# Kernel tuning notes

Measured on AMD Instinct MI355X. Metric: run time of the kernel, lower is better.

The kernel has to match this reference:

```python
import jax, jax.numpy as jnp
import numpy as np


def _lin(x, w, b=None):
    # torch nn.Linear convention: y = x @ W^T + b, W: (out, in)
    y = jnp.einsum('...d,ed->...e', x, w)
    return y + b if b is not None else y


def setup_inputs() -> dict:
    key = jax.random.key(0)
    B, N, M, d = 8, 256, 128, 128
    ks = jax.random.split(key, 20)
    sc = 1.0 / np.sqrt(d)
    inp = {
        's': jax.random.normal(ks[0], (B, N, d), jnp.float32),
        'v': jax.random.normal(ks[1], (B, N, M, d), jnp.float32),
        'gs': jax.random.normal(ks[2], (B, d), jnp.float32),
        'gv': jax.random.normal(ks[3], (B, M, d), jnp.float32),
        'gv2': jax.random.normal(ks[4], (B, M, M, d), jnp.float32),
        'lin1_w': jax.random.normal(ks[5], (d, d), jnp.float32) * sc,
        'lin1_b': jax.random.normal(ks[6], (d,), jnp.float32) * sc,
        'lin2_w': jax.random.normal(ks[7], (d, d), jnp.float32) * sc,
        'lin2_b': jax.random.normal(ks[8], (d,), jnp.float32) * sc,
        'lin3_w': jax.random.normal(ks[9], (d, d), jnp.float32) * sc,
        'lin3_b': jax.random.normal(ks[10], (d,), jnp.float32) * sc,
        'linv1_w': jax.random.normal(ks[11], (d, d), jnp.float32) * sc,
        'linv2_w': jax.random.normal(ks[12], (d, d), jnp.float32) * sc,
        'linv3_w': jax.random.normal(ks[13], (d, d), jnp.float32) * sc,
        'mlp_w1': jax.random.normal(ks[14], (d, d), jnp.float32) * sc,
        'mlp_b1': jax.random.normal(ks[15], (d,), jnp.float32) * sc,
        'mlp_w2': jax.random.normal(ks[16], (d, d), jnp.float32) * sc,
        'mlp_b2': jax.random.normal(ks[17], (d,), jnp.float32) * sc,
    }
    return inp


def reference(s, v, gs, gv, gv2,
              lin1_w, lin1_b, lin2_w, lin2_b, lin3_w, lin3_b,
              linv1_w, linv2_w, linv3_w,
              mlp_w1, mlp_b1, mlp_w2, mlp_b2):
    # v update: three (B,N,M,d) branches, averaged
    v_vv2 = _lin(jnp.einsum('bnmd,bmcd->bncd', v, gv2), linv1_w)
    v_vs = _lin(gs[:, None, None, :] * v, linv3_w)
    v_sv = _lin(s[:, :, None, :] * gv[:, None, :, :], linv2_w)
    v_new = (v_vv2 + v_sv + v_vs) / 3
    # s update
    s_v2t = jnp.einsum('bmmd->bd', gv2)                 # per-channel trace of gv2
    s_vv = jnp.einsum('bmd,bnmd->bnd', gv, v_new)
    s_new = ((_lin(s_v2t, lin1_w, lin1_b) * gs)[:, None, :]
             * _lin(s, lin2_w, lin2_b)
             * _lin(s_vv, lin3_w, lin3_b))
    # MLP: Linear -> ReLU -> Linear
    s_new = _lin(jax.nn.relu(_lin(s_new, mlp_w1, mlp_b1)), mlp_w2, mlp_b2)
    return (s_new, v_new)
```

## Files before the change

### kernel.cpp

```cpp
#include <hip/hip_runtime.h>
#include <hip/hip_bf16.h>
#include <stdint.h>

#define B_ 8
#define N_ 256
#define M_ 128
#define D_ 128

typedef __attribute__((ext_vector_type(8))) short short8;
typedef __attribute__((ext_vector_type(4))) short short4v;
typedef __attribute__((ext_vector_type(4))) float f32x4;

static __device__ __forceinline__ unsigned short f2bf(float x) {
    union { float f; unsigned int u; } c; c.f = x;
    unsigned int r = (c.u + 0x7FFFu + ((c.u >> 16) & 1u)) >> 16;
    return (unsigned short)r;
}
static __device__ __forceinline__ unsigned short bfhu(float x) {
    union { float f; unsigned int u; } c; c.f = x;
    return (unsigned short)((c.u + 0x8000u) >> 16);
}
static __device__ __forceinline__ unsigned int pkhu(float a, float b) {
    union { float f; unsigned int u; } ca, cb; ca.f = a; cb.f = b;
    return ((ca.u + 0x8000u) >> 16) | ((cb.u + 0x8000u) & 0xFFFF0000u);
}
static __device__ __forceinline__ float4 mul4(float4 a, float4 b) {
    return make_float4(a.x * b.x, a.y * b.y, a.z * b.z, a.w * b.w);
}
static __device__ __forceinline__ short8 pack8(float4 a, float4 b) {
    return (short8){(short)f2bf(a.x), (short)f2bf(a.y), (short)f2bf(a.z), (short)f2bf(a.w),
                    (short)f2bf(b.x), (short)f2bf(b.y), (short)f2bf(b.z), (short)f2bf(b.w)};
}

__global__ void k0a_prep(const float* __restrict__ lin2_w, const float* __restrict__ lin3_w,
                         const float* __restrict__ mlp_w1, const float* __restrict__ mlp_w2,
                         const float* __restrict__ linv1_w, const float* __restrict__ linv2_w,
                         const float* __restrict__ linv3_w,
                         float* __restrict__ wT2, float* __restrict__ wT3,
                         float* __restrict__ wTm1, float* __restrict__ wTm2,
                         unsigned short* __restrict__ wfrag) {
    int gid = blockIdx.x * 256 + threadIdx.x;
    int task = gid >> 14;
    int idx = gid & 16383;
    if (task < 4) {
        int e = idx & 127, dd = idx >> 7;
        const float* src = task == 0 ? lin2_w : task == 1 ? lin3_w : task == 2 ? mlp_w1 : mlp_w2;
        float* dst = task == 0 ? wT2 : task == 1 ? wT3 : task == 2 ? wTm1 : wTm2;
        dst[dd * 128 + e] = src[e * 128 + dd];
    } else {
        int mat = task - 4;
        const float* src = mat == 0 ? linv1_w : mat == 1 ? linv2_w : linv3_w;
        int e = idx >> 7, k = idx & 127;
        int dst = ((((e >> 4) * 12 + (mat * 4 + (k >> 5))) * 4 + ((k >> 3) & 3)) * 16 + (e & 15)) * 8
                  + (k & 7);
        wfrag[dst] = f2bf(src[idx] * (1.0f / 3.0f));
    }
}

__global__ void k0b_trace(const float* __restrict__ gv2, float* __restrict__ s_v2t) {
    int b = blockIdx.x, d = threadIdx.x;
    const float* p = gv2 + (size_t)b * (M_ * M_ * D_) + d;
    float acc = 0.f;
    #pragma unroll 8
    for (int m = 0; m < 128; ++m) acc += p[(size_t)m * 16512];
    s_v2t[b * 128 + d] = acc;
}

__global__ void k0c_g1(const float* __restrict__ s_v2t, const float* __restrict__ lin1_w,
                       const float* __restrict__ lin1_b, const float* __restrict__ gs,
                       float* __restrict__ g1) {
    __shared__ float sv[128];
    int b = blockIdx.x, e = threadIdx.x;
    sv[e] = s_v2t[b * 128 + e];
    __syncthreads();
    const float* w = lin1_w + e * 128;
    float acc = 0.f;
    #pragma unroll 4
    for (int dd = 0; dd < 128; ++dd) acc = fmaf(sv[dd], w[dd], acc);
    g1[b * 128 + e] = (acc + lin1_b[e]) * gs[b * 128 + e];
}

__global__ __launch_bounds__(256) void kt_v(const float* __restrict__ v,
                                            unsigned short* __restrict__ vT) {
    __shared__ unsigned short tl[128 * 136];
    int bid = blockIdx.x;
    int b = bid >> 8;
    int R0 = (bid & 255) * 128;
    int t = threadIdx.x;
    const float* src = v + ((size_t)b * 32768 + R0) * 128;
    #pragma unroll
    for (int i = 0; i < 16; ++i) {
        int flat = i * 256 + t;
        int row = flat >> 5, slot = flat & 31;
        float4 x = *(const float4*)(src + (size_t)row * 128 + slot * 4);
        #pragma unroll
        for (int j = 0; j < 4; ++j) {
            int d = slot * 4 + j;
            tl[d * 136 + (row ^ (((d >> 2) & 7) << 3))] = bfhu(((const float*)&x)[j]);
        }
    }
    __syncthreads();
    #pragma unroll
    for (int i = 0; i < 8; ++i) {
        int flat = i * 256 + t;
        int d = flat >> 4, rs = flat & 15;
        short8 y = *(const short8*)&tl[d * 136 + ((rs * 8) ^ (((d >> 2) & 7) << 3))];
        *(short8*)(vT + (size_t)(b * 128 + d) * 32768 + R0 + rs * 8) = y;
    }
}

__global__ __launch_bounds__(256) void kt_g(const float* __restrict__ gv2,
                                            unsigned short* __restrict__ gT) {
    __shared__ unsigned short tl[128 * 136];
    int bid = blockIdx.x;
    int b = bid >> 7;
    int c = bid & 127;
    int t = threadIdx.x;
    const float* src = gv2 + ((size_t)(b * 128) * 128 + c) * 128;
    #pragma unroll
    for (int i = 0; i < 16; ++i) {
        int flat = i * 256 + t;
        int m = flat >> 5, slot = flat & 31;
        float4 x = *(const float4*)(src + (size_t)m * 16384 + slot * 4);
        #pragma unroll
        for (int j = 0; j < 4; ++j) {
            int d = slot * 4 + j;
            tl[d * 136 + (m ^ (((d >> 2) & 7) << 3))] = bfhu(((const float*)&x)[j]);
        }
    }
    __syncthreads();
    #pragma unroll
    for (int i = 0; i < 8; ++i) {
        int flat = i * 256 + t;
        int d = flat >> 4, ms = flat & 15;
        short8 y = *(const short8*)&tl[d * 136 + ((ms * 8) ^ (((d >> 2) & 7) << 3))];
        *(short8*)(gT + ((size_t)(b * 128 + d) * 128 + c) * 128 + ms * 8) = y;
    }
}

__global__ __launch_bounds__(512, 2) void k1_T2_fast(const unsigned short* __restrict__ vT,
                                                     const unsigned short* __restrict__ gT,
                                                     unsigned short* __restrict__ t2base) {
    __shared__ unsigned short sm[40960];
    int bid = blockIdx.x;
    int b = bid & 7;
    int r = bid >> 3;
    int nt = r & 3, ch = (r >> 2) & 1, dc = r >> 3;
    int n0 = nt * 64, c0 = ch * 64, d0 = dc * 8;
    int t = threadIdx.x;
    int w = t >> 6, lane = t & 63, ln15 = lane & 15, kg = lane >> 4;

    f32x4 acc[4][4];
    #pragma unroll
    for (int i = 0; i < 4; ++i)
        #pragma unroll
        for (int j = 0; j < 4; ++j) acc[i][j] = (f32x4){0.f, 0.f, 0.f, 0.f};

    for (int mc = 0; mc < 4; ++mc) {
        int m0 = mc * 32;
        #pragma unroll
        for (int i = 0; i < 4; ++i) {
            int flat = i * 512 + t;
            int d = flat >> 8, x = (flat >> 2) & 63, ms = flat & 3;
            short8 a = *(const short8*)(vT + ((size_t)(b * 128 + d0 + d) * 256 + n0 + x) * 128
                                           + m0 + ms * 8);
            *(short8*)&sm[d * 2560 + x * 40 + ms * 8] = a;
            short8 g = *(const short8*)(gT + ((size_t)(b * 128 + d0 + d) * 128 + c0 + x) * 128
                                           + m0 + ms * 8);
            *(short8*)&sm[20480 + d * 2560 + x * 40 + ms * 8] = g;
        }
        __syncthreads();
        short8 af[4], bf[4];
        #pragma unroll
        for (int i = 0; i < 4; ++i)
            af[i] = *(const short8*)&sm[w * 2560 + (i * 16 + ln15) * 40 + kg * 8];
        #pragma unroll
        for (int j = 0; j < 4; ++j)
            bf[j] = *(const short8*)&sm[20480 + w * 2560 + (j * 16 + ln15) * 40 + kg * 8];
        #pragma unroll
        for (int i = 0; i < 4; ++i)
            #pragma unroll
            for (int j = 0; j < 4; ++j)
                acc[i][j] = __builtin_amdgcn_mfma_f32_16x16x32_bf16(af[i], bf[j], acc[i][j], 0, 0, 0);
        __syncthreads();
    }
    #pragma unroll
    for (int i = 0; i < 4; ++i)
        #pragma unroll
        for (int j = 0; j < 4; ++j)
            #pragma unroll
            for (int q = 0; q < 4; ++q) {
                int n = i * 16 + kg * 4 + q;
                int c = j * 16 + ln15;
                sm[n * 520 + c * 8 + w] = bfhu(acc[i][j][q]);
            }
    __syncthreads();
    #pragma unroll
    for (int p = 0; p < 8; ++p) {
        int u = p * 512 + t;
        int n = u >> 6;
        int c = u & 63;
        short8 x = *(const short8*)&sm[n * 520 + c * 8];
        size_t kb = (size_t)(b * N_ + n0 + n) * 2 + ch;
        *(short8*)(t2base + kb * 16384 + (size_t)((c >> 4) * 16 + dc) * 128 + (c & 15) * 8) = x;
    }
}

__global__ __launch_bounds__(512, 4) void k1_T2_legacy(const float* __restrict__ v,
                                                       const float* __restrict__ gv2,
                                                       unsigned short* __restrict__ t2base) {
    __shared__ unsigned short sm[40960];
    int bid = blockIdx.x;
    int b = bid & 7;
    int r = bid >> 3;
    int nt = r & 3, ch = (r >> 2) & 1, dc = r >> 3;
    int n0 = nt * 64, c0 = ch * 64, d0 = dc * 8;
    int t = threadIdx.x;
    int w = t >> 6, lane = t & 63, ln15 = lane & 15, kg = lane >> 4;

    f32x4 acc[4][4];
    #pragma unroll
    for (int i = 0; i < 4; ++i)
        #pragma unroll
        for (int j = 0; j < 4; ++j) acc[i][j] = (f32x4){0.f, 0.f, 0.f, 0.f};

    int d0l = (t & 1) * 4;
    int am = (t >> 1) & 31, anb = t >> 6;
    int bc = (t >> 1) & 63, bmb = t >> 7;

    for (int mc = 0; mc < 4; ++mc) {
        int m0 = mc * 32;
        {
            const float* src = v + (((size_t)(b * N_ + n0) * M_ + m0 + am) * D_ + d0 + d0l);
            #pragma unroll
            for (int p = 0; p < 8; ++p) {
                int n = p * 8 + anb;
                float4 x = *(const float4*)(src + (size_t)n * (M_ * D_));
                #pragma unroll
                for (int j = 0; j < 4; ++j)
                    sm[(d0l + j) * 2560 + n * 40 + am] = f2bf(((const float*)&x)[j]);
            }
        }
        {
            const float* src = gv2 + (((size_t)(b * M_ + m0) * M_ + c0 + bc) * D_ + d0 + d0l);
            #pragma unroll
            for (int p = 0; p < 8; ++p) {
                int m = p * 4 + bmb;
                float4 x = *(const float4*)(src + (size_t)m * (M_ * D_));
                #pragma unroll
                for (int j = 0; j < 4; ++j)
                    sm[20480 + (d0l + j) * 2560 + bc * 40 + m] = f2bf(((const float*)&x)[j]);
            }
        }
        __syncthreads();
        short8 af[4], bf[4];
        #pragma unroll
        for (int i = 0; i < 4; ++i)
            af[i] = *(const short8*)&sm[w * 2560 + (i * 16 + ln15) * 40 + kg * 8];
        #pragma unroll
        for (int j = 0; j < 4; ++j)
            bf[j] = *(const short8*)&sm[20480 + w * 2560 + (j * 16 + ln15) * 40 + kg * 8];
        #pragma unroll
        for (int i = 0; i < 4; ++i)
            #pragma unroll
            for (int j = 0; j < 4; ++j)
                acc[i][j] = __builtin_amdgcn_mfma_f32_16x16x32_bf16(af[i], bf[j], acc[i][j], 0, 0, 0);
        __syncthreads();
    }
    #pragma unroll
    for (int i = 0; i < 4; ++i)
        #pragma unroll
        for (int j = 0; j < 4; ++j)
            #pragma unroll
            for (int q = 0; q < 4; ++q) {
                int n = i * 16 + kg * 4 + q;
                int c = j * 16 + ln15;
                sm[(n * 64 + c) * 8 + w] = f2bf(acc[i][j][q]);
            }
    __syncthreads();
    #pragma unroll
    for (int p = 0; p < 8; ++p) {
        int u = p * 512 + t;
        int n = u >> 6;
        int c = u & 63;
        short8 x = *(const short8*)&sm[(n * 64 + c) * 8];
        size_t kb = (size_t)(b * N_ + n0 + n) * 2 + ch;
        *(short8*)(t2base + kb * 16384 + (size_t)((c >> 4) * 16 + dc) * 128 + (c & 15) * 8) = x;
    }
}

__global__ __launch_bounds__(512, 2) void k2_vnew(
        const float* __restrict__ s, const float* __restrict__ v,
        const float* __restrict__ gs, const float* __restrict__ gv,
        const unsigned short* __restrict__ wfrag,
        float* __restrict__ vnew, float* __restrict__ svv) {
    __shared__ unsigned short smw[49152];
    __shared__ float part[2][4][128];
    int t = threadIdx.x;
    int w = t >> 6;
    int sb = w >> 2;
    int w4 = w & 3;
    int kb2 = blockIdx.x * 2 + sb;
    int b = kb2 >> 8;
    int lane = t & 63, ln15 = lane & 15, kgrp = lane >> 4;

    #pragma unroll
    for (int r = 0; r < 12; ++r) {
        int idx = (r * 512 + t) * 8;
        *(short8*)&smw[idx] = *(const short8*)(wfrag + idx);
    }
    const unsigned short* t2u = (const unsigned short*)(vnew + (size_t)kb2 * 16384);
    short8 aT[2][4];
    #pragma unroll
    for (int h = 0; h < 2; ++h) {
        int rt = w4 * 2 + h;
        const unsigned short* tb = t2u + (rt >> 2) * 16384 + ((rt & 3) * 16 + kgrp) * 128 + ln15 * 8;
        #pragma unroll
        for (int kk = 0; kk < 4; ++kk)
            aT[h][kk] = *(const short8*)(tb + kk * 512);
    }
    const float* srow = s + (size_t)kb2 * 128;
    const float* gsr  = gs + (size_t)b * 128;
    float4 ss[8], qq[8];
    #pragma unroll
    for (int kk = 0; kk < 4; ++kk) {
        int dd = kk * 32 + kgrp * 8;
        ss[kk * 2]     = *(const float4*)(srow + dd);
        ss[kk * 2 + 1] = *(const float4*)(srow + dd + 4);
        qq[kk * 2]     = *(const float4*)(gsr + dd);
        qq[kk * 2 + 1] = *(const float4*)(gsr + dd + 4);
    }
    __syncthreads();

    float psum[8] = {0.f, 0.f, 0.f, 0.f, 0.f, 0.f, 0.f, 0.f};
    #pragma unroll
    for (int h = 0; h < 2; ++h) {
        int rt = w4 * 2 + h;
        int ca = rt * 16 + ln15;
        const float* gvr = gv + ((size_t)b * M_ + ca) * D_;
        const float* vr  = v + ((size_t)kb2 * M_ + ca) * D_;
        short8 aD[8];
        #pragma unroll
        for (int kk = 0; kk < 4; ++kk) {
            int dd = kk * 32 + kgrp * 8;
            float4 g0 = *(const float4*)(gvr + dd), g1 = *(const float4*)(gvr + dd + 4);
            float4 v0 = *(const float4*)(vr + dd),  v1 = *(const float4*)(vr + dd + 4);
            aD[kk]     = pack8(mul4(ss[kk * 2], g0), mul4(ss[kk * 2 + 1], g1));
            aD[4 + kk] = pack8(mul4(qq[kk * 2], v0), mul4(qq[kk * 2 + 1], v1));
        }
        float* outp = vnew + (size_t)kb2 * 16384 + (rt >> 2) * 8192;
        int rowl = (rt & 3) * 16 + kgrp * 4;
        const float* grow = gv + ((size_t)b * M_ + rt * 16 + kgrp * 4) * D_;
        #pragma unroll
        for (int ct = 0; ct < 8; ++ct) {
            f32x4 acc = {0.f, 0.f, 0.f, 0.f};
            #pragma unroll
            for (int kk = 0; kk < 12; ++kk) {
                short8 a = (kk < 4) ? aT[h][kk] : aD[kk - 4];
                short8 bfr = *(const short8*)&smw[(((ct * 12 + kk) * 4 + kgrp) * 16 + ln15) * 8];
                acc = __builtin_amdgcn_mfma_f32_16x16x32_bf16(a, bfr, acc, 0, 0, 0);
            }
            int e = ct * 16 + ln15;
            #pragma unroll
            for (int q = 0; q < 4; ++q) {
                outp[(size_t)(rowl + q) * 128 + e] = acc[q];
                psum[ct] = fmaf(grow[(size_t)q * 128 + e], acc[q], psum[ct]);
            }
        }
    }
    #pragma unroll
    for (int ct = 0; ct < 8; ++ct) {
        psum[ct] += __shfl_xor(psum[ct], 16);
        psum[ct] += __shfl_xor(psum[ct], 32);
    }
    if (kgrp == 0) {
        #pragma unroll
        for (int ct = 0; ct < 8; ++ct) part[sb][w4][ct * 16 + ln15] = psum[ct];
    }
    __syncthreads();
    int tl = t & 255;
    int sb2 = t >> 8;
    if (tl < 128) {
        int kbo = blockIdx.x * 2 + sb2;
        svv[(size_t)kbo * 128 + tl] =
            part[sb2][0][tl] + part[sb2][1][tl] + part[sb2][2][tl] + part[sb2][3][tl];
    }
}

__global__ __launch_bounds__(256) void k4_spath(
        const float* __restrict__ s, const float* __restrict__ svv,
        const float* __restrict__ g1,
        const float* __restrict__ wT2, const float* __restrict__ lin2_b,
        const float* __restrict__ wT3, const float* __restrict__ lin3_b,
        const float* __restrict__ wTm1, const float* __restrict__ mlp_b1,
        const float* __restrict__ wTm2, const float* __restrict__ mlp_b2,
        float* __restrict__ sout) {
    __shared__ float xs[8][128], xv[8][128], pre[8][128], hbuf[8][128];
    int t = threadIdx.x;
    int rowb = blockIdx.x * 8;
    int b = rowb >> 8;
    #pragma unroll
    for (int i = 0; i < 4; ++i) {
        int vi = i * 256 + t;
        int r = vi >> 7, dd = vi & 127;
        xs[r][dd] = s[(size_t)(rowb + r) * 128 + dd];
        xv[r][dd] = svv[(size_t)(rowb + r) * 128 + dd];
    }
    __syncthreads();
    int e = t & 127, h2 = t >> 7;
    float b2 = lin2_b[e], b3 = lin3_b[e], g1v = g1[b * 128 + e];
    float a2[4] = {b2, b2, b2, b2}, a3[4] = {b3, b3, b3, b3};
    for (int dd = 0; dd < 128; ++dd) {
        float w2 = wT2[dd * 128 + e], w3 = wT3[dd * 128 + e];
        #pragma unroll
        for (int r = 0; r < 4; ++r) {
            a2[r] = fmaf(xs[h2 * 4 + r][dd], w2, a2[r]);
            a3[r] = fmaf(xv[h2 * 4 + r][dd], w3, a3[r]);
        }
    }
    #pragma unroll
    for (int r = 0; r < 4; ++r) pre[h2 * 4 + r][e] = g1v * a2[r] * a3[r];
    __syncthreads();
    float bm1 = mlp_b1[e];
    float ah[4] = {bm1, bm1, bm1, bm1};
    for (int dd = 0; dd < 128; ++dd) {
        float w = wTm1[dd * 128 + e];
        #pragma unroll
        for (int r = 0; r < 4; ++r) ah[r] = fmaf(pre[h2 * 4 + r][dd], w, ah[r]);
    }
    #pragma unroll
    for (int r = 0; r < 4; ++r) hbuf[h2 * 4 + r][e] = fmaxf(ah[r], 0.f);
    __syncthreads();
    float bm2 = mlp_b2[e];
    float ao[4] = {bm2, bm2, bm2, bm2};
    for (int dd = 0; dd < 128; ++dd) {
        float w = wTm2[dd * 128 + e];
        #pragma unroll
        for (int r = 0; r < 4; ++r) ao[r] = fmaf(hbuf[h2 * 4 + r][dd], w, ao[r]);
    }
    #pragma unroll
    for (int r = 0; r < 4; ++r) sout[(size_t)(rowb + h2 * 4 + r) * 128 + e] = ao[r];
}

extern "C" void kernel_launch(void* const* d_in, const int* in_sizes, int n_in,
                              void* d_out, int out_size, void* d_ws, size_t ws_size,
                              hipStream_t stream) {
    const float* s       = (const float*)d_in[0];
    const float* v       = (const float*)d_in[1];
    const float* gs      = (const float*)d_in[2];
    const float* gv      = (const float*)d_in[3];
    const float* gv2     = (const float*)d_in[4];
    const float* lin1_w  = (const float*)d_in[5];
    const float* lin1_b  = (const float*)d_in[6];
    const float* lin2_w  = (const float*)d_in[7];
    const float* lin2_b  = (const float*)d_in[8];
    const float* lin3_w  = (const float*)d_in[9];
    const float* lin3_b  = (const float*)d_in[10];
    const float* linv1_w = (const float*)d_in[11];
    const float* linv2_w = (const float*)d_in[12];
    const float* linv3_w = (const float*)d_in[13];
    const float* mlp_w1  = (const float*)d_in[14];
    const float* mlp_b1  = (const float*)d_in[15];
    const float* mlp_w2  = (const float*)d_in[16];
    const float* mlp_b2  = (const float*)d_in[17];

    float* sout = (float*)d_out;
    float* vnew = (float*)d_out + 262144;

    float* wsf   = (float*)d_ws;
    float* wT2   = wsf;
    float* wT3   = wsf + 16384;
    float* wTm1  = wsf + 32768;
    float* wTm2  = wsf + 49152;
    float* s_v2t = wsf + 65536;
    float* g1    = wsf + 66560;
    float* svv   = wsf + 67584;
    unsigned short* wfrag = (unsigned short*)(wsf + 329728);
    unsigned short* vT = (unsigned short*)((char*)d_ws + 2097152);
    unsigned short* gT = (unsigned short*)((char*)d_ws + 69206016);
    bool big = ws_size >= 102760448ULL;

    k0a_prep<<<448, 256, 0, stream>>>(lin2_w, lin3_w, mlp_w1, mlp_w2,
                                      linv1_w, linv2_w, linv3_w,
                                      wT2, wT3, wTm1, wTm2, wfrag);
    k0b_trace<<<8, 128, 0, stream>>>(gv2, s_v2t);
    k0c_g1<<<8, 128, 0, stream>>>(s_v2t, lin1_w, lin1_b, gs, g1);
    if (big) {
        kt_v<<<2048, 256, 0, stream>>>(v, vT);
        kt_g<<<1024, 256, 0, stream>>>(gv2, gT);
        k1_T2_fast<<<1024, 512, 0, stream>>>(vT, gT, (unsigned short*)vnew);
    } else {
        k1_T2_legacy<<<1024, 512, 0, stream>>>(v, gv2, (unsigned short*)vnew);
    }
    k2_vnew<<<1024, 512, 0, stream>>>(s, v, gs, gv, wfrag, vnew, svv);
    k4_spath<<<256, 256, 0, stream>>>(s, svv, g1, wT2, lin2_b, wT3, lin3_b,
                                      wTm1, mlp_b1, wTm2, mlp_b2, sout);
}
```

Baseline: 263.2 us.

## Precompute bf16 gs*v in transpose kernel and use persistent k2 kernel

The v transpose kernel now also writes a bf16 copy of gs*v in row-major layout. A new persistent k2 variant loads the weight fragments into shared memory once per block and loops over four work pairs, reading the half-size bf16 gs*v instead of fp32 v. It only runs when the workspace is large enough. This aims to cut v read traffic in k2 and the repeated weight staging, at the cost of an extra 64MB bf16 write in kt_v and lower occupancy (256 blocks, launch bound 1).

New measurement: 276.8 us. 5.2% more time.

```diff
diff --git a/kernel.cpp b/kernel.cpp
--- a/kernel.cpp
+++ b/kernel.cpp
@@ -81,22 +81,31 @@
 }
 
 __global__ __launch_bounds__(256) void kt_v(const float* __restrict__ v,
-                                            unsigned short* __restrict__ vT) {
+                                            const float* __restrict__ gs,
+                                            unsigned short* __restrict__ vT,
+                                            unsigned short* __restrict__ vgs) {
     __shared__ unsigned short tl[128 * 136];
     int bid = blockIdx.x;
     int b = bid >> 8;
     int R0 = (bid & 255) * 128;
     int t = threadIdx.x;
+    int slot = t & 31;
     const float* src = v + ((size_t)b * 32768 + R0) * 128;
+    float4 gs4 = *(const float4*)(gs + b * 128 + slot * 4);
     #pragma unroll
     for (int i = 0; i < 16; ++i) {
         int flat = i * 256 + t;
-        int row = flat >> 5, slot = flat & 31;
+        int row = flat >> 5;
         float4 x = *(const float4*)(src + (size_t)row * 128 + slot * 4);
         #pragma unroll
         for (int j = 0; j < 4; ++j) {
             int d = slot * 4 + j;
             tl[d * 136 + (row ^ (((d >> 2) & 7) << 3))] = bfhu(((const float*)&x)[j]);
+        }
+        if (vgs) {
+            uint2 pg = make_uint2(pkhu(x.x * gs4.x, x.y * gs4.y),
+                                  pkhu(x.z * gs4.z, x.w * gs4.w));
+            *(uint2*)(vgs + ((size_t)b * 32768 + R0 + row) * 128 + slot * 4) = pg;
         }
     }
     __syncthreads();
@@ -286,6 +295,102 @@
         short8 x = *(const short8*)&sm[(n * 64 + c) * 8];
         size_t kb = (size_t)(b * N_ + n0 + n) * 2 + ch;
         *(short8*)(t2base + kb * 16384 + (size_t)((c >> 4) * 16 + dc) * 128 + (c & 15) * 8) = x;
+    }
+}
+
+__global__ __launch_bounds__(512, 1) void k2_vnew_p(
+        const float* __restrict__ s, const unsigned short* __restrict__ vgs,
+        const float* __restrict__ gv,
+        const unsigned short* __restrict__ wfrag,
+        float* __restrict__ vnew, float* __restrict__ svv) {
+    __shared__ unsigned short smw[49152];
+    __shared__ float part[2][4][128];
+    int t = threadIdx.x;
+    int w = t >> 6, sb = w >> 2, w4 = w & 3;
+    int lane = t & 63, ln15 = lane & 15, kgrp = lane >> 4;
+
+    #pragma unroll
+    for (int r = 0; r < 12; ++r) {
+        int idx = (r * 512 + t) * 8;
+        *(short8*)&smw[idx] = *(const short8*)(wfrag + idx);
+    }
+
+    for (int j = 0; j < 4; ++j) {
+        int pair = blockIdx.x + 256 * j;
+        int kb2 = pair * 2 + sb;
+        int b = kb2 >> 8;
+        const unsigned short* t2u = (const unsigned short*)(vnew + (size_t)kb2 * 16384);
+        short8 aT[2][4];
+        #pragma unroll
+        for (int h = 0; h < 2; ++h) {
+            int rt = w4 * 2 + h;
+            const unsigned short* tb = t2u + (rt >> 2) * 16384 + ((rt & 3) * 16 + kgrp) * 128
+                                      + ln15 * 8;
+            #pragma unroll
+            for (int kk = 0; kk < 4; ++kk)
+                aT[h][kk] = *(const short8*)(tb + kk * 512);
+        }
+        const float* srow = s + (size_t)kb2 * 128;
+        float4 ss[8];
+        #pragma unroll
+        for (int kk = 0; kk < 4; ++kk) {
+            int dd = kk * 32 + kgrp * 8;
+            ss[kk * 2]     = *(const float4*)(srow + dd);
+            ss[kk * 2 + 1] = *(const float4*)(srow + dd + 4);
+        }
+        __syncthreads();
+
+        float psum[8] = {0.f, 0.f, 0.f, 0.f, 0.f, 0.f, 0.f, 0.f};
+        #pragma unroll
+        for (int h = 0; h < 2; ++h) {
+            int rt = w4 * 2 + h;
+            int ca = rt * 16 + ln15;
+            const float* gvr = gv + ((size_t)b * M_ + ca) * D_;
+            const unsigned short* vgr = vgs + ((size_t)kb2 * M_ + ca) * D_;
+            short8 aD[8];
+            #pragma unroll
+            for (int kk = 0; kk < 4; ++kk) {
+                int dd = kk * 32 + kgrp * 8;
+                float4 g0 = *(const float4*)(gvr + dd), g1 = *(const float4*)(gvr + dd + 4);
+                aD[kk]     = pack8(mul4(ss[kk * 2], g0), mul4(ss[kk * 2 + 1], g1));
+                aD[4 + kk] = *(const short8*)(vgr + dd);
+            }
+            float* outp = vnew + (size_t)kb2 * 16384 + (rt >> 2) * 8192;
+            int rowl = (rt & 3) * 16 + kgrp * 4;
+            const float* grow = gv + ((size_t)b * M_ + rt * 16 + kgrp * 4) * D_;
+            #pragma unroll
+            for (int ct = 0; ct < 8; ++ct) {
+                f32x4 acc = {0.f, 0.f, 0.f, 0.f};
+                #pragma unroll
+                for (int kk = 0; kk < 12; ++kk) {
+                    short8 a = (kk < 4) ? aT[h][kk] : aD[kk - 4];
+                    short8 bfr = *(const short8*)&smw[(((ct * 12 + kk) * 4 + kgrp) * 16 + ln15) * 8];
+                    acc = __builtin_amdgcn_mfma_f32_16x16x32_bf16(a, bfr, acc, 0, 0, 0);
+                }
+                int e = ct * 16 + ln15;
+                #pragma unroll
+                for (int q = 0; q < 4; ++q) {
+                    outp[(size_t)(rowl + q) * 128 + e] = acc[q];
+                    psum[ct] = fmaf(grow[(size_t)q * 128 + e], acc[q], psum[ct]);
+                }
+            }
+        }
+        #pragma unroll
+        for (int ct = 0; ct < 8; ++ct) {
+            psum[ct] += __shfl_xor(psum[ct], 16);
+            psum[ct] += __shfl_xor(psum[ct], 32);
+        }
+        if (kgrp == 0) {
+            #pragma unroll
+            for (int ct = 0; ct < 8; ++ct) part[sb][w4][ct * 16 + ln15] = psum[ct];
+        }
+        __syncthreads();
+        int tl = t & 255, sb2 = t >> 8;
+        if (tl < 128) {
+            int kbo = pair * 2 + sb2;
+            svv[(size_t)kbo * 128 + tl] =
+                part[sb2][0][tl] + part[sb2][1][tl] + part[sb2][2][tl] + part[sb2][3][tl];
+        }
     }
 }
 
@@ -476,9 +581,11 @@
     float* g1    = wsf + 66560;
     float* svv   = wsf + 67584;
     unsigned short* wfrag = (unsigned short*)(wsf + 329728);
-    unsigned short* vT = (unsigned short*)((char*)d_ws + 2097152);
-    unsigned short* gT = (unsigned short*)((char*)d_ws + 69206016);
-    bool big = ws_size >= 102760448ULL;
+    unsigned short* vT  = (unsigned short*)((char*)d_ws + 2097152);
+    unsigned short* gT  = (unsigned short*)((char*)d_ws + 69206016);
+    unsigned short* vgs = (unsigned short*)((char*)d_ws + 102760448);
+    bool big  = ws_size >= 102760448ULL;
+    bool huge = ws_size >= 169869312ULL;
 
     k0a_prep<<<448, 256, 0, stream>>>(lin2_w, lin3_w, mlp_w1, mlp_w2,
                                       linv1_w, linv2_w, linv3_w,
@@ -486,13 +593,17 @@
     k0b_trace<<<8, 128, 0, stream>>>(gv2, s_v2t);
     k0c_g1<<<8, 128, 0, stream>>>(s_v2t, lin1_w, lin1_b, gs, g1);
     if (big) {
-        kt_v<<<2048, 256, 0, stream>>>(v, vT);
+        kt_v<<<2048, 256, 0, stream>>>(v, gs, vT, huge ? vgs : (unsigned short*)nullptr);
         kt_g<<<1024, 256, 0, stream>>>(gv2, gT);
         k1_T2_fast<<<1024, 512, 0, stream>>>(vT, gT, (unsigned short*)vnew);
     } else {
         k1_T2_legacy<<<1024, 512, 0, stream>>>(v, gv2, (unsigned short*)vnew);
     }
-    k2_vnew<<<1024, 512, 0, stream>>>(s, v, gs, gv, wfrag, vnew, svv);
+    if (huge) {
+        k2_vnew_p<<<256, 512, 0, stream>>>(s, vgs, gv, wfrag, vnew, svv);
+    } else {
+        k2_vnew<<<1024, 512, 0, stream>>>(s, v, gs, gv, wfrag, vnew, svv);
+    }
     k4_spath<<<256, 256, 0, stream>>>(s, svv, g1, wT2, lin2_b, wT3, lin3_b,
                                       wTm1, mlp_b1, wTm2, mlp_b2, sout);
 }
```

## Restructure v_new kernel to keep weight fragments in registers and stage A in LDS

Applied to the files above, without the earlier changes.

The v_new projection kernel is rewritten so each block handles a single (b,n) row. Each wave owns one 16-wide output column tile and keeps its 12 weight fragments in registers, so the 96KB LDS weight copy goes away. The A operands (the T2 tile plus the s·gv and gs·v products) are now built cooperatively in a small LDS buffer, one row tile at a time. Row tiles are processed in a permuted order so that reading the in-place T2 buffer does not collide with writing v_new. The aim is higher occupancy and less LDS pressure, at the cost of two barriers per row tile and twice as many blocks.

Result: no change. 258.9 us (-1.6%).

```diff
diff --git a/kernel.cpp b/kernel.cpp
--- a/kernel.cpp
+++ b/kernel.cpp
@@ -23,13 +23,6 @@
 static __device__ __forceinline__ unsigned int pkhu(float a, float b) {
     union { float f; unsigned int u; } ca, cb; ca.f = a; cb.f = b;
     return ((ca.u + 0x8000u) >> 16) | ((cb.u + 0x8000u) & 0xFFFF0000u);
-}
-static __device__ __forceinline__ float4 mul4(float4 a, float4 b) {
-    return make_float4(a.x * b.x, a.y * b.y, a.z * b.z, a.w * b.w);
-}
-static __device__ __forceinline__ short8 pack8(float4 a, float4 b) {
-    return (short8){(short)f2bf(a.x), (short)f2bf(a.y), (short)f2bf(a.z), (short)f2bf(a.w),
-                    (short)f2bf(b.x), (short)f2bf(b.y), (short)f2bf(b.z), (short)f2bf(b.w)};
 }
 
 __global__ void k0a_prep(const float* __restrict__ lin2_w, const float* __restrict__ lin3_w,
@@ -289,102 +282,77 @@
     }
 }
 
-__global__ __launch_bounds__(512, 2) void k2_vnew(
+__global__ __launch_bounds__(512, 4) void k2_vnew_w(
         const float* __restrict__ s, const float* __restrict__ v,
         const float* __restrict__ gs, const float* __restrict__ gv,
         const unsigned short* __restrict__ wfrag,
         float* __restrict__ vnew, float* __restrict__ svv) {
-    __shared__ unsigned short smw[49152];
-    __shared__ float part[2][4][128];
-    int t = threadIdx.x;
-    int w = t >> 6;
-    int sb = w >> 2;
-    int w4 = w & 3;
-    int kb2 = blockIdx.x * 2 + sb;
+    __shared__ unsigned short lds_a[6144];
+    int t = threadIdx.x;
+    int kb2 = blockIdx.x;
     int b = kb2 >> 8;
-    int lane = t & 63, ln15 = lane & 15, kgrp = lane >> 4;
-
-    #pragma unroll
-    for (int r = 0; r < 12; ++r) {
-        int idx = (r * 512 + t) * 8;
-        *(short8*)&smw[idx] = *(const short8*)(wfrag + idx);
-    }
+    int w = t >> 6, lane = t & 63, ln15 = lane & 15, kgrp = lane >> 4;
+    int ct = w;
+
+    f32x4 wreg[12];
+    #pragma unroll
+    for (int kk = 0; kk < 12; ++kk)
+        wreg[kk] = *(const f32x4*)&wfrag[(((ct * 12 + kk) * 4 + kgrp) * 16 + ln15) * 8];
+    asm volatile("" : "+v"(wreg[0]), "+v"(wreg[1]), "+v"(wreg[2]), "+v"(wreg[3]),
+                      "+v"(wreg[4]), "+v"(wreg[5]), "+v"(wreg[6]), "+v"(wreg[7]),
+                      "+v"(wreg[8]), "+v"(wreg[9]), "+v"(wreg[10]), "+v"(wreg[11]));
+
+    int r_s = t >> 5;
+    int q5 = t & 31;
+    int dd0 = q5 * 4;
+    float4 s4  = *(const float4*)(s + (size_t)kb2 * 128 + dd0);
+    float4 gs4 = *(const float4*)(gs + (size_t)b * 128 + dd0);
+    const float* gvb = gv + (size_t)b * 16384;
     const unsigned short* t2u = (const unsigned short*)(vnew + (size_t)kb2 * 16384);
-    short8 aT[2][4];
-    #pragma unroll
-    for (int h = 0; h < 2; ++h) {
-        int rt = w4 * 2 + h;
-        const unsigned short* tb = t2u + (rt >> 2) * 16384 + ((rt & 3) * 16 + kgrp) * 128 + ln15 * 8;
-        #pragma unroll
-        for (int kk = 0; kk < 4; ++kk)
-            aT[h][kk] = *(const short8*)(tb + kk * 512);
-    }
-    const float* srow = s + (size_t)kb2 * 128;
-    const float* gsr  = gs + (size_t)b * 128;
-    float4 ss[8], qq[8];
-    #pragma unroll
-    for (int kk = 0; kk < 4; ++kk) {
-        int dd = kk * 32 + kgrp * 8;
-        ss[kk * 2]     = *(const float4*)(srow + dd);
-        ss[kk * 2 + 1] = *(const float4*)(srow + dd + 4);
-        qq[kk * 2]     = *(const float4*)(gsr + dd);
-        qq[kk * 2 + 1] = *(const float4*)(gsr + dd + 4);
-    }
-    __syncthreads();
-
-    float psum[8] = {0.f, 0.f, 0.f, 0.f, 0.f, 0.f, 0.f, 0.f};
-    #pragma unroll
-    for (int h = 0; h < 2; ++h) {
-        int rt = w4 * 2 + h;
-        int ca = rt * 16 + ln15;
-        const float* gvr = gv + ((size_t)b * M_ + ca) * D_;
-        const float* vr  = v + ((size_t)kb2 * M_ + ca) * D_;
-        short8 aD[8];
-        #pragma unroll
-        for (int kk = 0; kk < 4; ++kk) {
-            int dd = kk * 32 + kgrp * 8;
-            float4 g0 = *(const float4*)(gvr + dd), g1 = *(const float4*)(gvr + dd + 4);
-            float4 v0 = *(const float4*)(vr + dd),  v1 = *(const float4*)(vr + dd + 4);
-            aD[kk]     = pack8(mul4(ss[kk * 2], g0), mul4(ss[kk * 2 + 1], g1));
-            aD[4 + kk] = pack8(mul4(qq[kk * 2], v0), mul4(qq[kk * 2 + 1], v1));
-        }
-        float* outp = vnew + (size_t)kb2 * 16384 + (rt >> 2) * 8192;
-        int rowl = (rt & 3) * 16 + kgrp * 4;
-        const float* grow = gv + ((size_t)b * M_ + rt * 16 + kgrp * 4) * D_;
-        #pragma unroll
-        for (int ct = 0; ct < 8; ++ct) {
-            f32x4 acc = {0.f, 0.f, 0.f, 0.f};
-            #pragma unroll
-            for (int kk = 0; kk < 12; ++kk) {
-                short8 a = (kk < 4) ? aT[h][kk] : aD[kk - 4];
-                short8 bfr = *(const short8*)&smw[(((ct * 12 + kk) * 4 + kgrp) * 16 + ln15) * 8];
-                acc = __builtin_amdgcn_mfma_f32_16x16x32_bf16(a, bfr, acc, 0, 0, 0);
-            }
-            int e = ct * 16 + ln15;
-            #pragma unroll
-            for (int q = 0; q < 4; ++q) {
-                outp[(size_t)(rowl + q) * 128 + e] = acc[q];
-                psum[ct] = fmaf(grow[(size_t)q * 128 + e], acc[q], psum[ct]);
-            }
-        }
-    }
-    #pragma unroll
-    for (int ct = 0; ct < 8; ++ct) {
-        psum[ct] += __shfl_xor(psum[ct], 16);
-        psum[ct] += __shfl_xor(psum[ct], 32);
-    }
-    if (kgrp == 0) {
-        #pragma unroll
-        for (int ct = 0; ct < 8; ++ct) part[sb][w4][ct * 16 + ln15] = psum[ct];
-    }
-    __syncthreads();
-    int tl = t & 255;
-    int sb2 = t >> 8;
-    if (tl < 128) {
-        int kbo = blockIdx.x * 2 + sb2;
-        svv[(size_t)kbo * 128 + tl] =
-            part[sb2][0][tl] + part[sb2][1][tl] + part[sb2][2][tl] + part[sb2][3][tl];
-    }
+    float* outp = vnew + (size_t)kb2 * 16384;
+    int lw = 2048 + (q5 >> 3) * 512 + ((q5 >> 1) & 3) * 128 + r_s * 8 + (q5 & 1) * 4;
+
+    float psum = 0.f;
+    #pragma unroll
+    for (int j = 0; j < 8; ++j) {
+        int rt = (0x45760132u >> (4 * j)) & 7;
+        int crow = (rt >> 2) * 64 + (rt & 3) * 16;
+        if (t < 256) {
+            short8 x = *(const short8*)(t2u + (rt >> 2) * 16384 + (rt & 3) * 2048 + t * 8);
+            *(short8*)&lds_a[t * 8] = x;
+        }
+        {
+            float4 g4 = *(const float4*)(gvb + (size_t)(crow + r_s) * 128 + dd0);
+            uint2 p = make_uint2(pkhu(s4.x * g4.x, s4.y * g4.y),
+                                 pkhu(s4.z * g4.z, s4.w * g4.w));
+            *(uint2*)&lds_a[lw] = p;
+        }
+        {
+            float4 v4 = *(const float4*)(v + ((size_t)kb2 * 128 + crow + r_s) * 128 + dd0);
+            uint2 p = make_uint2(pkhu(gs4.x * v4.x, gs4.y * v4.y),
+                                 pkhu(gs4.z * v4.z, gs4.w * v4.w));
+            *(uint2*)&lds_a[lw + 2048] = p;
+        }
+        __syncthreads();
+        f32x4 acc = {0.f, 0.f, 0.f, 0.f};
+        #pragma unroll
+        for (int kk = 0; kk < 12; ++kk) {
+            short8 a = *(const short8*)&lds_a[kk * 512 + kgrp * 128 + ln15 * 8];
+            acc = __builtin_amdgcn_mfma_f32_16x16x32_bf16(
+                a, __builtin_bit_cast(short8, wreg[kk]), acc, 0, 0, 0);
+        }
+        int e = ct * 16 + ln15;
+        #pragma unroll
+        for (int q = 0; q < 4; ++q) {
+            int row = crow + kgrp * 4 + q;
+            outp[(size_t)row * 128 + e] = acc[q];
+            psum = fmaf(gvb[(size_t)row * 128 + e], acc[q], psum);
+        }
+        __syncthreads();
+    }
+    psum += __shfl_xor(psum, 16);
+    psum += __shfl_xor(psum, 32);
+    if (kgrp == 0) svv[(size_t)kb2 * 128 + ct * 16 + ln15] = psum;
 }
 
 __global__ __launch_bounds__(256) void k4_spath(
@@ -476,8 +444,8 @@
     float* g1    = wsf + 66560;
     float* svv   = wsf + 67584;
     unsigned short* wfrag = (unsigned short*)(wsf + 329728);
-    unsigned short* vT = (unsigned short*)((char*)d_ws + 2097152);
-    unsigned short* gT = (unsigned short*)((char*)d_ws + 69206016);
+    unsigned short* vT  = (unsigned short*)((char*)d_ws + 2097152);
+    unsigned short* gT  = (unsigned short*)((char*)d_ws + 69206016);
     bool big = ws_size >= 102760448ULL;
 
     k0a_prep<<<448, 256, 0, stream>>>(lin2_w, lin3_w, mlp_w1, mlp_w2,
@@ -492,7 +460,7 @@
     } else {
         k1_T2_legacy<<<1024, 512, 0, stream>>>(v, gv2, (unsigned short*)vnew);
     }
-    k2_vnew<<<1024, 512, 0, stream>>>(s, v, gs, gv, wfrag, vnew, svv);
+    k2_vnew_w<<<2048, 512, 0, stream>>>(s, v, gs, gv, wfrag, vnew, svv);
     k4_spath<<<256, 256, 0, stream>>>(s, svv, g1, wT2, lin2_b, wT3, lin3_b,
                                       wTm1, mlp_b1, wTm2, mlp_b2, sout);
 }
```
